# Kernel optimization log

Hardware: AMD Instinct MI355X
Metric: run time of the kernel (lower is better)

Reference implementation:

```python
import jax, jax.numpy as jnp
import numpy as np

B, S, D, H, FF = 1, 2048, 2048, 32, 8192
HD = D // H
SCALING = HD ** -0.5
WBITS, ABITS = 8, 8
NEG = jnp.finfo(jnp.float32).min


def ste_round(x):
    # straight-through estimator round
    return x + jax.lax.stop_gradient(jnp.round(x) - x)


def fake_quant(x, bits, axis):
    # min-max asymmetric fake quantization (OmniQuant-style dynamic quant)
    qmax = float(2 ** bits - 1)
    xmin = jnp.minimum(jnp.min(x, axis=axis, keepdims=True), 0.0)
    xmax = jnp.maximum(jnp.max(x, axis=axis, keepdims=True), 0.0)
    scale = jnp.maximum((xmax - xmin) / qmax, 1e-5)
    zp = jnp.round(-xmin / scale)
    q = jnp.clip(ste_round(x / scale) + zp, 0.0, qmax)
    return (q - zp) * scale


def qlinear(x, W, b):
    # QuantLinear: quantize activation per-token, weight per-output-channel
    xq = fake_quant(x, ABITS, -1)
    Wq = fake_quant(W, WBITS, 1)  # W: [out, in], per-row (output channel)
    return xq @ Wq.T + b


def layernorm(x, g, b):
    mu = jnp.mean(x, axis=-1, keepdims=True)
    var = jnp.var(x, axis=-1, keepdims=True)
    return (x - mu) * jax.lax.rsqrt(var + 1e-5) * g + b


def setup_inputs():
    key = jax.random.key(0)
    ks = jax.random.split(key, 16)
    w = lambda k, shape: (jax.random.normal(k, shape) * 0.02).astype(jnp.float32)
    hidden_states = jax.random.normal(ks[0], (B, S, D), dtype=jnp.float32)
    causal = jnp.tril(jnp.ones((S, S), dtype=bool))
    attention_mask = jnp.where(causal, 0.0, NEG)[None, None].astype(jnp.float32)
    attention_mask = jnp.broadcast_to(attention_mask, (B, 1, S, S))
    return {
        'hidden_states': hidden_states,
        'attention_mask': attention_mask,
        'Wq': w(ks[1], (D, D)), 'bq': jnp.zeros((D,), jnp.float32),
        'Wk': w(ks[2], (D, D)), 'bk': jnp.zeros((D,), jnp.float32),
        'Wv': w(ks[3], (D, D)), 'bv': jnp.zeros((D,), jnp.float32),
        'Wo': w(ks[4], (D, D)), 'bo': jnp.zeros((D,), jnp.float32),
        'ln1_g': jnp.ones((D,), jnp.float32), 'ln1_b': jnp.zeros((D,), jnp.float32),
        'W1': w(ks[5], (FF, D)), 'b1': jnp.zeros((FF,), jnp.float32),
        'W2': w(ks[6], (D, FF)), 'b2': jnp.zeros((D,), jnp.float32),
        'ln2_g': jnp.ones((D,), jnp.float32), 'ln2_b': jnp.zeros((D,), jnp.float32),
    }


def _split_heads(x):
    # [B,S,D] -> [B,H,S,HD]
    return x.reshape(B, S, H, HD).transpose(0, 2, 1, 3)


def _layer(hidden_states, attention_mask, Wq, bq, Wk, bk, Wv, bv, Wo, bo,
           ln1_g, ln1_b, W1, b1, W2, b2, ln2_g, ln2_b):
    # ---- self attention block (do_layer_norm_before=True) ----
    residual = hidden_states
    x = layernorm(hidden_states, ln1_g, ln1_b)

    q = qlinear(x, Wq, bq) * SCALING
    q = fake_quant(q, ABITS, -1)          # qkt_matmul.quant_x1
    k = qlinear(x, Wk, bk)
    k = fake_quant(k, ABITS, -1)          # qkt_matmul.quant_x2
    v = qlinear(x, Wv, bv)
    v = fake_quant(v, ABITS, -1)          # pv_matmul.quant_x2

    qh, kh, vh = _split_heads(q), _split_heads(k), _split_heads(v)
    scores = jnp.einsum('bhqd,bhkd->bhqk', qh, kh)  # [B,H,S,S]
    scores = scores + attention_mask
    scores = jnp.maximum(scores, NEG)
    probs = jax.nn.softmax(scores, axis=-1)
    probs = fake_quant(probs, ABITS, -1)  # pv_matmul.quant_x1
    ctx = jnp.einsum('bhqk,bhkd->bhqd', probs, vh)
    ctx = ctx.transpose(0, 2, 1, 3).reshape(B, S, D)
    attn_out = qlinear(ctx, Wo, bo)
    hidden_states = residual + attn_out

    # ---- FFN block ----
    residual = hidden_states
    x = layernorm(hidden_states, ln2_g, ln2_b)
    x = jax.nn.relu(qlinear(x, W1, b1))
    x = qlinear(x, W2, b2)
    return residual + x


def reference(hidden_states, attention_mask, Wq, bq, Wk, bk, Wv, bv, Wo, bo,
              ln1_g, ln1_b, W1, b1, W2, b2, ln2_g, ln2_b):
    return _layer(hidden_states, attention_mask, Wq, bq, Wk, bk, Wv, bv, Wo, bo,
                  ln1_g, ln1_b, W1, b1, W2, b2, ln2_g, ln2_b)
```

## Files before the change

kernel.cpp:

```cpp
#include <hip/hip_runtime.h>
#include <hip/hip_bf16.h>
#include <math.h>

#define S_LEN 2048
#define D_DIM 2048
#define H_NUM 32
#define HD_DIM 64
#define FF_DIM 8192
#define QMAX 255.0f
#define LOG2E 1.4426950408889634f

typedef __attribute__((ext_vector_type(4))) float f32x4;
typedef __attribute__((ext_vector_type(4))) int i32x4;
typedef __attribute__((ext_vector_type(8))) __bf16 bf16x8;
typedef unsigned short u16;
typedef signed char i8;

__device__ __forceinline__ u16 f32i_to_bf16(float v) {
  return (u16)(__float_as_uint(v) >> 16);
}
__device__ __forceinline__ u16 f32_to_bf16_rne(float v) {
  __bf16 b = (__bf16)v;
  return *(u16*)&b;
}
__device__ __forceinline__ float bf16_to_f32(u16 u) {
  return __uint_as_float((unsigned int)u << 16);
}
__device__ __forceinline__ int pack4_i8(float q0, float q1, float q2, float q3) {
  int c0 = (int)q0 - 128, c1 = (int)q1 - 128, c2 = (int)q2 - 128, c3 = (int)q3 - 128;
  return (c0 & 0xFF) | ((c1 & 0xFF) << 8) | ((c2 & 0xFF) << 16) | ((c3 & 0xFF) << 24);
}

__device__ __forceinline__ float wred_sum(float v) {
#pragma unroll
  for (int o = 1; o < 64; o <<= 1) v += __shfl_xor(v, o, 64);
  return v;
}
__device__ __forceinline__ float wred_min(float v) {
#pragma unroll
  for (int o = 1; o < 64; o <<= 1) v = fminf(v, __shfl_xor(v, o, 64));
  return v;
}
__device__ __forceinline__ float wred_max(float v) {
#pragma unroll
  for (int o = 1; o < 64; o <<= 1) v = fmaxf(v, __shfl_xor(v, o, 64));
  return v;
}

__device__ __forceinline__ void gload_lds16(const void* g, void* l) {
  __builtin_amdgcn_global_load_lds(
      (__attribute__((address_space(1))) void*)(g),
      (__attribute__((address_space(3))) void*)(l), 16, 0, 0);
}

__device__ __forceinline__ void xcd_swz(int& bx, int& by) {
  const int gy = gridDim.y;
  const int nwg = gridDim.x * gy;
  const int orig = blockIdx.y + gy * blockIdx.x;
  const int swz = (orig & 7) * (nwg >> 3) + (orig >> 3);
  by = swz % gy;
  bx = swz / gy;
}

__device__ __forceinline__ void attn_map(int bid, int& h, int& ti) {
  h = bid & (H_NUM - 1);
  const int a = (bid >> 5) & 7;
  const int b = bid >> 8;
  ti = (b == 0) ? (31 - a) : (b == 1) ? a : (b == 2) ? (23 - a) : (8 + a);
}

__global__ __launch_bounds__(256) void ln_quant_i8(const float* __restrict__ x,
                                                   const float* __restrict__ g,
                                                   const float* __restrict__ bvec,
                                                   i8* __restrict__ out,
                                                   float* __restrict__ srow,
                                                   float* __restrict__ zrow,
                                                   float* __restrict__ S0row,
                                                   float* __restrict__ S1row) {
  __shared__ float red[8];
  const int row = blockIdx.x, tid = threadIdx.x;
  const float4* xr = (const float4*)(x + (size_t)row * D_DIM);
  const float4* g4 = (const float4*)g;
  const float4* b4 = (const float4*)bvec;

  float4 v0 = xr[tid], v1 = xr[tid + 256];
  float s = v0.x + v0.y + v0.z + v0.w + v1.x + v1.y + v1.z + v1.w;
  float ss = v0.x * v0.x + v0.y * v0.y + v0.z * v0.z + v0.w * v0.w +
             v1.x * v1.x + v1.y * v1.y + v1.z * v1.z + v1.w * v1.w;
  s = wred_sum(s); ss = wred_sum(ss);
  if ((tid & 63) == 0) { red[tid >> 6] = s; red[4 + (tid >> 6)] = ss; }
  __syncthreads();
  float mu = (red[0] + red[1] + red[2] + red[3]) / (float)D_DIM;
  float var = (red[4] + red[5] + red[6] + red[7]) / (float)D_DIM - mu * mu;
  float rstd = 1.0f / sqrtf(var + 1e-5f);
  __syncthreads();

  float mn = 0.f, mx = 0.f;
  float4 n0, n1;
  {
    float4 gg = g4[tid], bb = b4[tid];
    n0.x = (v0.x - mu) * rstd * gg.x + bb.x; n0.y = (v0.y - mu) * rstd * gg.y + bb.y;
    n0.z = (v0.z - mu) * rstd * gg.z + bb.z; n0.w = (v0.w - mu) * rstd * gg.w + bb.w;
    gg = g4[tid + 256]; bb = b4[tid + 256];
    n1.x = (v1.x - mu) * rstd * gg.x + bb.x; n1.y = (v1.y - mu) * rstd * gg.y + bb.y;
    n1.z = (v1.z - mu) * rstd * gg.z + bb.z; n1.w = (v1.w - mu) * rstd * gg.w + bb.w;
    mn = fminf(mn, fminf(fminf(n0.x, n0.y), fminf(n0.z, n0.w)));
    mn = fminf(mn, fminf(fminf(n1.x, n1.y), fminf(n1.z, n1.w)));
    mx = fmaxf(mx, fmaxf(fmaxf(n0.x, n0.y), fmaxf(n0.z, n0.w)));
    mx = fmaxf(mx, fmaxf(fmaxf(n1.x, n1.y), fmaxf(n1.z, n1.w)));
  }
  mn = wred_min(mn); mx = wred_max(mx);
  if ((tid & 63) == 0) { red[tid >> 6] = mn; red[4 + (tid >> 6)] = mx; }
  __syncthreads();
  mn = fminf(fminf(red[0], red[1]), fminf(red[2], red[3]));
  mx = fmaxf(fmaxf(red[4], red[5]), fmaxf(red[6], red[7]));
  float scale = fmaxf((mx - mn) / QMAX, 1e-5f);
  float zp = rintf(-mn / scale);
  if (tid == 0) { srow[row] = scale; zrow[row] = 128.0f - zp; }

  float q00 = fminf(fmaxf(rintf(n0.x / scale) + zp, 0.f), QMAX);
  float q01 = fminf(fmaxf(rintf(n0.y / scale) + zp, 0.f), QMAX);
  float q02 = fminf(fmaxf(rintf(n0.z / scale) + zp, 0.f), QMAX);
  float q03 = fminf(fmaxf(rintf(n0.w / scale) + zp, 0.f), QMAX);
  float q10 = fminf(fmaxf(rintf(n1.x / scale) + zp, 0.f), QMAX);
  float q11 = fminf(fmaxf(rintf(n1.y / scale) + zp, 0.f), QMAX);
  float q12 = fminf(fmaxf(rintf(n1.z / scale) + zp, 0.f), QMAX);
  float q13 = fminf(fmaxf(rintf(n1.w / scale) + zp, 0.f), QMAX);
  *(int*)&out[(size_t)row * D_DIM + tid * 4] = pack4_i8(q00, q01, q02, q03);
  *(int*)&out[(size_t)row * D_DIM + 1024 + tid * 4] = pack4_i8(q10, q11, q12, q13);
  float s0 = q00 + q01 + q02 + q03 - 512.f;
  float s1 = q10 + q11 + q12 + q13 - 512.f;
  __syncthreads();
  s0 = wred_sum(s0); s1 = wred_sum(s1);
  if ((tid & 63) == 0) { red[tid >> 6] = s0; red[4 + (tid >> 6)] = s1; }
  __syncthreads();
  if (tid == 0) {
    S0row[row] = red[0] + red[1] + red[2] + red[3];
    S1row[row] = red[4] + red[5] + red[6] + red[7];
  }
}

__global__ __launch_bounds__(256) void act_quant_i8(const float* __restrict__ x,
                                                    i8* __restrict__ out,
                                                    float* __restrict__ srow,
                                                    float* __restrict__ zrow,
                                                    float* __restrict__ S0row,
                                                    float* __restrict__ S1row) {
  __shared__ float red[8];
  const int row = blockIdx.x, tid = threadIdx.x;
  const float4* xr = (const float4*)(x + (size_t)row * D_DIM);
  float4 n0 = xr[tid], n1 = xr[tid + 256];
  float mn = 0.f, mx = 0.f;
  mn = fminf(mn, fminf(fminf(n0.x, n0.y), fminf(n0.z, n0.w)));
  mn = fminf(mn, fminf(fminf(n1.x, n1.y), fminf(n1.z, n1.w)));
  mx = fmaxf(mx, fmaxf(fmaxf(n0.x, n0.y), fmaxf(n0.z, n0.w)));
  mx = fmaxf(mx, fmaxf(fmaxf(n1.x, n1.y), fmaxf(n1.z, n1.w)));
  mn = wred_min(mn); mx = wred_max(mx);
  if ((tid & 63) == 0) { red[tid >> 6] = mn; red[4 + (tid >> 6)] = mx; }
  __syncthreads();
  mn = fminf(fminf(red[0], red[1]), fminf(red[2], red[3]));
  mx = fmaxf(fmaxf(red[4], red[5]), fmaxf(red[6], red[7]));
  float scale = fmaxf((mx - mn) / QMAX, 1e-5f);
  float zp = rintf(-mn / scale);
  if (tid == 0) { srow[row] = scale; zrow[row] = 128.0f - zp; }
  float q00 = fminf(fmaxf(rintf(n0.x / scale) + zp, 0.f), QMAX);
  float q01 = fminf(fmaxf(rintf(n0.y / scale) + zp, 0.f), QMAX);
  float q02 = fminf(fmaxf(rintf(n0.z / scale) + zp, 0.f), QMAX);
  float q03 = fminf(fmaxf(rintf(n0.w / scale) + zp, 0.f), QMAX);
  float q10 = fminf(fmaxf(rintf(n1.x / scale) + zp, 0.f), QMAX);
  float q11 = fminf(fmaxf(rintf(n1.y / scale) + zp, 0.f), QMAX);
  float q12 = fminf(fmaxf(rintf(n1.z / scale) + zp, 0.f), QMAX);
  float q13 = fminf(fmaxf(rintf(n1.w / scale) + zp, 0.f), QMAX);
  *(int*)&out[(size_t)row * D_DIM + tid * 4] = pack4_i8(q00, q01, q02, q03);
  *(int*)&out[(size_t)row * D_DIM + 1024 + tid * 4] = pack4_i8(q10, q11, q12, q13);
  float s0 = q00 + q01 + q02 + q03 - 512.f;
  float s1 = q10 + q11 + q12 + q13 - 512.f;
  __syncthreads();
  s0 = wred_sum(s0); s1 = wred_sum(s1);
  if ((tid & 63) == 0) { red[tid >> 6] = s0; red[4 + (tid >> 6)] = s1; }
  __syncthreads();
  if (tid == 0) {
    S0row[row] = red[0] + red[1] + red[2] + red[3];
    S1row[row] = red[4] + red[5] + red[6] + red[7];
  }
}

__device__ __forceinline__ void wquantD_body(const float* __restrict__ wr0,
                                             i8* __restrict__ wo,
                                             float* __restrict__ sc,
                                             float* __restrict__ zc,
                                             float* __restrict__ S0c,
                                             float* __restrict__ S1c, int row) {
  __shared__ float red[8];
  const int tid = threadIdx.x;
  const float4* wr = (const float4*)wr0;
  float4 v0 = wr[tid], v1 = wr[tid + 256];
  float mn = 0.f, mx = 0.f;
  mn = fminf(mn, fminf(fminf(v0.x, v0.y), fminf(v0.z, v0.w)));
  mn = fminf(mn, fminf(fminf(v1.x, v1.y), fminf(v1.z, v1.w)));
  mx = fmaxf(mx, fmaxf(fmaxf(v0.x, v0.y), fmaxf(v0.z, v0.w)));
  mx = fmaxf(mx, fmaxf(fmaxf(v1.x, v1.y), fmaxf(v1.z, v1.w)));
  mn = wred_min(mn); mx = wred_max(mx);
  if ((tid & 63) == 0) { red[tid >> 6] = mn; red[4 + (tid >> 6)] = mx; }
  __syncthreads();
  mn = fminf(fminf(red[0], red[1]), fminf(red[2], red[3]));
  mx = fmaxf(fmaxf(red[4], red[5]), fmaxf(red[6], red[7]));
  float scale = fmaxf((mx - mn) / QMAX, 1e-5f);
  float zp = rintf(-mn / scale);
  if (tid == 0) { sc[row] = scale; zc[row] = 128.0f - zp; }
  float q00 = fminf(fmaxf(rintf(v0.x / scale) + zp, 0.f), QMAX);
  float q01 = fminf(fmaxf(rintf(v0.y / scale) + zp, 0.f), QMAX);
  float q02 = fminf(fmaxf(rintf(v0.z / scale) + zp, 0.f), QMAX);
  float q03 = fminf(fmaxf(rintf(v0.w / scale) + zp, 0.f), QMAX);
  float q10 = fminf(fmaxf(rintf(v1.x / scale) + zp, 0.f), QMAX);
  float q11 = fminf(fmaxf(rintf(v1.y / scale) + zp, 0.f), QMAX);
  float q12 = fminf(fmaxf(rintf(v1.z / scale) + zp, 0.f), QMAX);
  float q13 = fminf(fmaxf(rintf(v1.w / scale) + zp, 0.f), QMAX);
  *(int*)&wo[tid * 4] = pack4_i8(q00, q01, q02, q03);
  *(int*)&wo[1024 + tid * 4] = pack4_i8(q10, q11, q12, q13);
  float s0 = q00 + q01 + q02 + q03 - 512.f;
  float s1 = q10 + q11 + q12 + q13 - 512.f;
  __syncthreads();
  s0 = wred_sum(s0); s1 = wred_sum(s1);
  if ((tid & 63) == 0) { red[tid >> 6] = s0; red[4 + (tid >> 6)] = s1; }
  __syncthreads();
  if (tid == 0) {
    S0c[row] = red[0] + red[1] + red[2] + red[3];
    S1c[row] = red[4] + red[5] + red[6] + red[7];
  }
}

__global__ __launch_bounds__(256) void wquantD_i8(
    const float* __restrict__ Wq, i8* __restrict__ Oq, float* sq_, float* zq_, float* aq_, float* bq_,
    const float* __restrict__ Wk, i8* __restrict__ Ok, float* sk_, float* zk_, float* ak_, float* bk_,
    const float* __restrict__ Wv, i8* __restrict__ Ov, float* sv_, float* zv_, float* av_, float* bv_,
    const float* __restrict__ Wo, i8* __restrict__ Oo, float* so_, float* zo_, float* ao_, float* bo_,
    const float* __restrict__ W1, i8* __restrict__ O1, float* s1_, float* z1_, float* a1_, float* b1_) {
  const int b = blockIdx.x;
  int which, row;
  if (b < 4 * D_DIM) { which = b >> 11; row = b & (D_DIM - 1); }
  else { which = 4; row = b - 4 * D_DIM; }
  const float* W = (which == 0) ? Wq : (which == 1) ? Wk : (which == 2) ? Wv : (which == 3) ? Wo : W1;
  i8* O = (which == 0) ? Oq : (which == 1) ? Ok : (which == 2) ? Ov : (which == 3) ? Oo : O1;
  float* sc = (which == 0) ? sq_ : (which == 1) ? sk_ : (which == 2) ? sv_ : (which == 3) ? so_ : s1_;
  float* zc = (which == 0) ? zq_ : (which == 1) ? zk_ : (which == 2) ? zv_ : (which == 3) ? zo_ : z1_;
  float* Sa = (which == 0) ? aq_ : (which == 1) ? ak_ : (which == 2) ? av_ : (which == 3) ? ao_ : a1_;
  float* Sb = (which == 0) ? bq_ : (which == 1) ? bk_ : (which == 2) ? bv_ : (which == 3) ? bo_ : b1_;
  wquantD_body(W + (size_t)row * D_DIM, O + (size_t)row * D_DIM, sc, zc, Sa, Sb, row);
}

__global__ __launch_bounds__(256) void wquantW2_i8(const float* __restrict__ W,
                                                   i8* __restrict__ Wi,
                                                   float* __restrict__ sc,
                                                   float* __restrict__ zc,
                                                   float* __restrict__ S0c,
                                                   float* __restrict__ S1c) {
  __shared__ float red[8];
  const int row = blockIdx.x, tid = threadIdx.x;
  const float4* wr = (const float4*)(W + (size_t)row * FF_DIM);
  float4 v[8];
#pragma unroll
  for (int j = 0; j < 8; ++j) v[j] = wr[tid + 256 * j];
  float mn = 0.f, mx = 0.f;
#pragma unroll
  for (int j = 0; j < 8; ++j) {
    mn = fminf(mn, fminf(fminf(v[j].x, v[j].y), fminf(v[j].z, v[j].w)));
    mx = fmaxf(mx, fmaxf(fmaxf(v[j].x, v[j].y), fmaxf(v[j].z, v[j].w)));
  }
  mn = wred_min(mn); mx = wred_max(mx);
  if ((tid & 63) == 0) { red[tid >> 6] = mn; red[4 + (tid >> 6)] = mx; }
  __syncthreads();
  mn = fminf(fminf(red[0], red[1]), fminf(red[2], red[3]));
  mx = fmaxf(fmaxf(red[4], red[5]), fmaxf(red[6], red[7]));
  float scale = fmaxf((mx - mn) / QMAX, 1e-5f);
  float zp = rintf(-mn / scale);
  if (tid == 0) { sc[row] = scale; zc[row] = 128.0f - zp; }
  float s0 = 0.f, s1 = 0.f;
#pragma unroll
  for (int j = 0; j < 8; ++j) {
    float q0 = fminf(fmaxf(rintf(v[j].x / scale) + zp, 0.f), QMAX);
    float q1 = fminf(fmaxf(rintf(v[j].y / scale) + zp, 0.f), QMAX);
    float q2 = fminf(fmaxf(rintf(v[j].z / scale) + zp, 0.f), QMAX);
    float q3 = fminf(fmaxf(rintf(v[j].w / scale) + zp, 0.f), QMAX);
    *(int*)&Wi[(size_t)row * FF_DIM + (tid + 256 * j) * 4] = pack4_i8(q0, q1, q2, q3);
    float gs = q0 + q1 + q2 + q3 - 512.f;
    if (j < 4) s0 += gs; else s1 += gs;
  }
  __syncthreads();
  s0 = wred_sum(s0); s1 = wred_sum(s1);
  if ((tid & 63) == 0) { red[tid >> 6] = s0; red[4 + (tid >> 6)] = s1; }
  __syncthreads();
  if (tid == 0) {
    S0c[row] = red[0] + red[1] + red[2] + red[3];
    S1c[row] = red[4] + red[5] + red[6] + red[7];
  }
}

__global__ __launch_bounds__(256) void requant3(
    const u16* __restrict__ qv, const float* __restrict__ tqmn, const float* __restrict__ tqmx,
    u16* __restrict__ qo, float* __restrict__ sqv,
    const u16* __restrict__ kv, const float* __restrict__ tkmn, const float* __restrict__ tkmx,
    u16* __restrict__ ko, float* __restrict__ skv,
    const u16* __restrict__ vv, const float* __restrict__ tvmn, const float* __restrict__ tvmx,
    u16* __restrict__ vo) {
// ... 314 lines not shown
    const int col = col0 + ni * 16;
#pragma unroll
    for (int mi = 0; mi < 4; ++mi)
#pragma unroll
      for (int r = 0; r < 4; ++r)
        dst[(size_t)(rbase + mi * 16 + r) * D_DIM + col] = (float)acc[mi][ni][r];
  }
}

__global__ __launch_bounds__(256) void splitk_reduce4(
    const float* __restrict__ part,
    const float* __restrict__ sxa, const float* __restrict__ zxa,
    const float* __restrict__ Sxa0, const float* __restrict__ Sxa1,
    const float* __restrict__ sw, const float* __restrict__ zw,
    const float* __restrict__ Sw0, const float* __restrict__ Sw1,
    float Kf, const float* __restrict__ bias, const float* __restrict__ res,
    float* __restrict__ out) {
  const size_t st4 = (size_t)S_LEN * D_DIM / 4;
  for (size_t i = (size_t)blockIdx.x * 256 + threadIdx.x; i < st4;
       i += (size_t)gridDim.x * 256) {
    const int row = (int)(i >> 9);
    const int c4 = (int)(i & 511);
    float4 s = ((const float4*)part)[i];
    float4 p1 = ((const float4*)part)[i + st4];
    float4 p2 = ((const float4*)part)[i + 2 * st4];
    float4 p3 = ((const float4*)part)[i + 3 * st4];
    s.x += p1.x + p2.x + p3.x; s.y += p1.y + p2.y + p3.y;
    s.z += p1.z + p2.z + p3.z; s.w += p1.w + p2.w + p3.w;
    const float sxr = sxa[row], zxr = zxa[row];
    const float Sxr = Sxa0[row] + Sxa1[row];
    float4 ws = ((const float4*)sw)[c4];
    float4 wz = ((const float4*)zw)[c4];
    float4 w0 = ((const float4*)Sw0)[c4];
    float4 w1 = ((const float4*)Sw1)[c4];
    float4 b4 = ((const float4*)bias)[c4];
    float4 o;
    o.x = sxr * ws.x * (s.x + zxr * (w0.x + w1.x) + wz.x * Sxr + Kf * zxr * wz.x) + b4.x;
    o.y = sxr * ws.y * (s.y + zxr * (w0.y + w1.y) + wz.y * Sxr + Kf * zxr * wz.y) + b4.y;
    o.z = sxr * ws.z * (s.z + zxr * (w0.z + w1.z) + wz.z * Sxr + Kf * zxr * wz.z) + b4.z;
    o.w = sxr * ws.w * (s.w + zxr * (w0.w + w1.w) + wz.w * Sxr + Kf * zxr * wz.w) + b4.w;
    if (res) {
      float4 r = ((const float4*)res)[i];
      o.x += r.x; o.y += r.y; o.z += r.z; o.w += r.w;
    }
    ((float4*)out)[i] = o;
  }
}

__global__ __launch_bounds__(256) void splitk_reduce_ln(
    const float* __restrict__ part,
    const float* __restrict__ sxa, const float* __restrict__ zxa,
    const float* __restrict__ Sxa0, const float* __restrict__ Sxa1,
    const float* __restrict__ sw, const float* __restrict__ zw,
    const float* __restrict__ Sw0, const float* __restrict__ Sw1,
    const float* __restrict__ bias, const float* __restrict__ res,
    float* __restrict__ h2out,
    const float* __restrict__ g, const float* __restrict__ bvec,
    i8* __restrict__ out, float* __restrict__ srow, float* __restrict__ zrow,
    float* __restrict__ S0row, float* __restrict__ S1row) {
  __shared__ float red[8];
  const int row = blockIdx.x, tid = threadIdx.x;
  const size_t st = (size_t)S_LEN * D_DIM;
  const float4* p0 = (const float4*)(part + (size_t)row * D_DIM);
  const float4* p1 = (const float4*)(part + st + (size_t)row * D_DIM);
  const float4* p2 = (const float4*)(part + 2 * st + (size_t)row * D_DIM);
  const float4* p3 = (const float4*)(part + 3 * st + (size_t)row * D_DIM);
  const float4* rr = (const float4*)(res + (size_t)row * D_DIM);
  const float4* b4 = (const float4*)bias;
  const float4* g4 = (const float4*)g;
  const float4* e4 = (const float4*)bvec;

  const float sxr = sxa[row], zxr = zxa[row];
  const float Sxr = Sxa0[row] + Sxa1[row];

  float4 v0, v1;
#pragma unroll
  for (int h = 0; h < 2; ++h) {
    const int idx = tid + h * 256;
    float4 a = p0[idx], q = p1[idx], u = p2[idx], w = p3[idx];
    float4 ws = ((const float4*)sw)[idx];
    float4 wz = ((const float4*)zw)[idx];
    float4 s0 = ((const float4*)Sw0)[idx];
    float4 s1 = ((const float4*)Sw1)[idx];
    float4 bb = b4[idx], rv = rr[idx];
    float4 o;
    o.x = sxr * ws.x * (a.x + q.x + u.x + w.x + zxr * (s0.x + s1.x) + wz.x * Sxr + 2048.0f * zxr * wz.x) + bb.x + rv.x;
    o.y = sxr * ws.y * (a.y + q.y + u.y + w.y + zxr * (s0.y + s1.y) + wz.y * Sxr + 2048.0f * zxr * wz.y) + bb.y + rv.y;
    o.z = sxr * ws.z * (a.z + q.z + u.z + w.z + zxr * (s0.z + s1.z) + wz.z * Sxr + 2048.0f * zxr * wz.z) + bb.z + rv.z;
    o.w = sxr * ws.w * (a.w + q.w + u.w + w.w + zxr * (s0.w + s1.w) + wz.w * Sxr + 2048.0f * zxr * wz.w) + bb.w + rv.w;
    if (h == 0) v0 = o; else v1 = o;
  }
  float* h2r = h2out + (size_t)row * D_DIM;
  *(float4*)&h2r[tid * 4] = v0;
  *(float4*)&h2r[1024 + tid * 4] = v1;

  float s = v0.x + v0.y + v0.z + v0.w + v1.x + v1.y + v1.z + v1.w;
  float ss = v0.x * v0.x + v0.y * v0.y + v0.z * v0.z + v0.w * v0.w +
             v1.x * v1.x + v1.y * v1.y + v1.z * v1.z + v1.w * v1.w;
  s = wred_sum(s); ss = wred_sum(ss);
  if ((tid & 63) == 0) { red[tid >> 6] = s; red[4 + (tid >> 6)] = ss; }
  __syncthreads();
  float mu = (red[0] + red[1] + red[2] + red[3]) / (float)D_DIM;
  float var = (red[4] + red[5] + red[6] + red[7]) / (float)D_DIM - mu * mu;
  float rstd = 1.0f / sqrtf(var + 1e-5f);
  __syncthreads();

  float mn = 0.f, mx = 0.f;
  float4 n0, n1;
  {
    float4 gg = g4[tid], bb = e4[tid];
    n0.x = (v0.x - mu) * rstd * gg.x + bb.x; n0.y = (v0.y - mu) * rstd * gg.y + bb.y;
    n0.z = (v0.z - mu) * rstd * gg.z + bb.z; n0.w = (v0.w - mu) * rstd * gg.w + bb.w;
    gg = g4[tid + 256]; bb = e4[tid + 256];
    n1.x = (v1.x - mu) * rstd * gg.x + bb.x; n1.y = (v1.y - mu) * rstd * gg.y + bb.y;
    n1.z = (v1.z - mu) * rstd * gg.z + bb.z; n1.w = (v1.w - mu) * rstd * gg.w + bb.w;
    mn = fminf(mn, fminf(fminf(n0.x, n0.y), fminf(n0.z, n0.w)));
    mn = fminf(mn, fminf(fminf(n1.x, n1.y), fminf(n1.z, n1.w)));
    mx = fmaxf(mx, fmaxf(fmaxf(n0.x, n0.y), fmaxf(n0.z, n0.w)));
    mx = fmaxf(mx, fmaxf(fmaxf(n1.x, n1.y), fmaxf(n1.z, n1.w)));
  }
  mn = wred_min(mn); mx = wred_max(mx);
  if ((tid & 63) == 0) { red[tid >> 6] = mn; red[4 + (tid >> 6)] = mx; }
  __syncthreads();
  mn = fminf(fminf(red[0], red[1]), fminf(red[2], red[3]));
  mx = fmaxf(fmaxf(red[4], red[5]), fmaxf(red[6], red[7]));
  float scale = fmaxf((mx - mn) / QMAX, 1e-5f);
  float zp = rintf(-mn / scale);
  if (tid == 0) { srow[row] = scale; zrow[row] = 128.0f - zp; }
  float q00 = fminf(fmaxf(rintf(n0.x / scale) + zp, 0.f), QMAX);
  float q01 = fminf(fmaxf(rintf(n0.y / scale) + zp, 0.f), QMAX);
  float q02 = fminf(fmaxf(rintf(n0.z / scale) + zp, 0.f), QMAX);
  float q03 = fminf(fmaxf(rintf(n0.w / scale) + zp, 0.f), QMAX);
  float q10 = fminf(fmaxf(rintf(n1.x / scale) + zp, 0.f), QMAX);
  float q11 = fminf(fmaxf(rintf(n1.y / scale) + zp, 0.f), QMAX);
  float q12 = fminf(fmaxf(rintf(n1.z / scale) + zp, 0.f), QMAX);
  float q13 = fminf(fmaxf(rintf(n1.w / scale) + zp, 0.f), QMAX);
  *(int*)&out[(size_t)row * D_DIM + tid * 4] = pack4_i8(q00, q01, q02, q03);
  *(int*)&out[(size_t)row * D_DIM + 1024 + tid * 4] = pack4_i8(q10, q11, q12, q13);
  float s0 = q00 + q01 + q02 + q03 - 512.f;
  float s1 = q10 + q11 + q12 + q13 - 512.f;
  __syncthreads();
  s0 = wred_sum(s0); s1 = wred_sum(s1);
  if ((tid & 63) == 0) { red[tid >> 6] = s0; red[4 + (tid >> 6)] = s1; }
  __syncthreads();
  if (tid == 0) {
    S0row[row] = red[0] + red[1] + red[2] + red[3];
    S1row[row] = red[4] + red[5] + red[6] + red[7];
  }
}

__global__ __launch_bounds__(256) void attn_ml(
    const u16* __restrict__ qi, const float* __restrict__ sq,
    const u16* __restrict__ ki, const float* __restrict__ sk,
    float* __restrict__ Mb, float* __restrict__ Lb) {
  __shared__ __align__(16) u16 Ks[64][72];
  int h, ti; attn_map(blockIdx.x, h, ti);
  const int i0 = ti * 64;
  const int tid = threadIdx.x;
  const int wid = tid >> 6, lane = tid & 63;
  const int lr = lane & 15, g = lane >> 4;
  const size_t hbase = (size_t)h * HD_DIM;

  const int r_a = tid >> 3, ch_a = tid & 7;
  const int r_b = 32 + r_a;

  const bf16x8 aq0 = *(const bf16x8*)&qi[(size_t)(i0 + wid * 16 + lr) * D_DIM + hbase + g * 8];
  const bf16x8 aq1 = *(const bf16x8*)&qi[(size_t)(i0 + wid * 16 + lr) * D_DIM + hbase + 32 + g * 8];
  float sq2[4];
#pragma unroll
  for (int r = 0; r < 4; ++r) sq2[r] = sq[i0 + wid * 16 + g * 4 + r] * LOG2E;

  const int ntiles = i0 / 64 + 1;
  float m_r[4] = {-1e30f, -1e30f, -1e30f, -1e30f};
  float l_r[4] = {0.f, 0.f, 0.f, 0.f};

  float4 ka0 = *(const float4*)&ki[(size_t)r_a * D_DIM + hbase + ch_a * 8];
  float4 ka1 = *(const float4*)&ki[(size_t)r_b * D_DIM + hbase + ch_a * 8];
  for (int t = 0; t < ntiles; ++t) {
    __syncthreads();
    *(float4*)&Ks[r_a][ch_a * 8] = ka0;
    *(float4*)&Ks[r_b][ch_a * 8] = ka1;
    __syncthreads();
    if (t + 1 < ntiles) {
      const int jn = (t + 1) * 64;
      ka0 = *(const float4*)&ki[(size_t)(jn + r_a) * D_DIM + hbase + ch_a * 8];
      ka1 = *(const float4*)&ki[(size_t)(jn + r_b) * D_DIM + hbase + ch_a * 8];
    }

    f32x4 accs[4] = {};
#pragma unroll
    for (int ni = 0; ni < 4; ++ni) {
      bf16x8 b0 = *(const bf16x8*)&Ks[ni * 16 + lr][g * 8];
      bf16x8 b1 = *(const bf16x8*)&Ks[ni * 16 + lr][32 + g * 8];
      accs[ni] = __builtin_amdgcn_mfma_f32_16x16x32_bf16(aq0, b0, accs[ni], 0, 0, 0);
      accs[ni] = __builtin_amdgcn_mfma_f32_16x16x32_bf16(aq1, b1, accs[ni], 0, 0, 0);
    }

    const int jt = t * 64;
    float tv[4][4];
#pragma unroll
    for (int ni = 0; ni < 4; ++ni) {
      const float skc = sk[jt + ni * 16 + lr];
#pragma unroll
      for (int r = 0; r < 4; ++r) tv[ni][r] = accs[ni][r] * sq2[r] * skc;
    }
    if (t == ntiles - 1) {
      const int jcol = jt + lr, irow = i0 + wid * 16 + g * 4;
#pragma unroll
      for (int ni = 0; ni < 4; ++ni)
#pragma unroll
        for (int r = 0; r < 4; ++r)
          if (jcol + ni * 16 > irow + r) tv[ni][r] = -1e30f;
    }
#pragma unroll
    for (int r = 0; r < 4; ++r) {
      float tmax = fmaxf(fmaxf(tv[0][r], tv[1][r]), fmaxf(tv[2][r], tv[3][r]));
      tmax = fmaxf(tmax, __shfl_xor(tmax, 1, 64));
      tmax = fmaxf(tmax, __shfl_xor(tmax, 2, 64));
      tmax = fmaxf(tmax, __shfl_xor(tmax, 4, 64));
      tmax = fmaxf(tmax, __shfl_xor(tmax, 8, 64));
      float mnew = fmaxf(m_r[r], tmax);
      float sum = exp2f(tv[0][r] - mnew) + exp2f(tv[1][r] - mnew) +
                  exp2f(tv[2][r] - mnew) + exp2f(tv[3][r] - mnew);
      sum += __shfl_xor(sum, 1, 64);
      sum += __shfl_xor(sum, 2, 64);
      sum += __shfl_xor(sum, 4, 64);
      sum += __shfl_xor(sum, 8, 64);
      l_r[r] = l_r[r] * exp2f(m_r[r] - mnew) + sum;
      m_r[r] = mnew;
    }
  }

  if (lr == 0) {
#pragma unroll
    for (int r = 0; r < 4; ++r) {
      const int row = i0 + wid * 16 + g * 4 + r;
      Mb[(size_t)h * S_LEN + row] = m_r[r];
      Lb[(size_t)h * S_LEN + row] = l_r[r];
    }
  }
}

__global__ __launch_bounds__(256) void attn_pv(
    const u16* __restrict__ qi, const float* __restrict__ sq,
    const u16* __restrict__ ki, const float* __restrict__ sk,
    const u16* __restrict__ vt,
    const float* __restrict__ Mb, const float* __restrict__ Lb,
    float* __restrict__ ctx) {
  __shared__ __align__(16) u16 Ks[64][72];
  __shared__ __align__(16) u16 Ps[64][72];
  __shared__ __align__(16) u16 Vt[64][72];
  int h, ti; attn_map(blockIdx.x, h, ti);
  const int i0 = ti * 64;
  const int tid = threadIdx.x;
  const int wid = tid >> 6, lane = tid & 63;
  const int lr = lane & 15, g = lane >> 4;
  const size_t hbase = (size_t)h * HD_DIM;
  const size_t vtbase = (size_t)h * HD_DIM * S_LEN;

  const int r_a = tid >> 3, ch_a = tid & 7;
  const int r_b = 32 + r_a;

  const bf16x8 aq0 = *(const bf16x8*)&qi[(size_t)(i0 + wid * 16 + lr) * D_DIM + hbase + g * 8];
  const bf16x8 aq1 = *(const bf16x8*)&qi[(size_t)(i0 + wid * 16 + lr) * D_DIM + hbase + 32 + g * 8];

  float sq2[4], b_r[4], qsc[4];
#pragma unroll
  for (int r = 0; r < 4; ++r) {
    const int row = i0 + wid * 16 + g * 4 + r;
    sq2[r] = sq[row] * LOG2E;
    float m_t = Mb[(size_t)h * S_LEN + row];
    float li = Lb[(size_t)h * S_LEN + row];
    float sc = fmaxf((1.0f / li) / QMAX, 1e-5f);
    qsc[r] = sc;
    b_r[r] = m_t - log2f(1.0f / (li * sc));
  }

  const int ntiles = i0 / 64 + 1;
  f32x4 acco[4] = {};
  float4 kb0 = *(const float4*)&ki[(size_t)r_a * D_DIM + hbase + ch_a * 8];
  float4 kb1 = *(const float4*)&ki[(size_t)r_b * D_DIM + hbase + ch_a * 8];
  float4 vb0 = *(const float4*)&vt[vtbase + (size_t)r_a * S_LEN + ch_a * 8];
  float4 vb1 = *(const float4*)&vt[vtbase + (size_t)r_b * S_LEN + ch_a * 8];
  for (int t = 0; t < ntiles; ++t) {
    __syncthreads();
    *(float4*)&Ks[r_a][ch_a * 8] = kb0;
    *(float4*)&Ks[r_b][ch_a * 8] = kb1;
    *(float4*)&Vt[r_a][ch_a * 8] = vb0;
    *(float4*)&Vt[r_b][ch_a * 8] = vb1;
    __syncthreads();
    if (t + 1 < ntiles) {
      const int jn = (t + 1) * 64;
      kb0 = *(const float4*)&ki[(size_t)(jn + r_a) * D_DIM + hbase + ch_a * 8];
      kb1 = *(const float4*)&ki[(size_t)(jn + r_b) * D_DIM + hbase + ch_a * 8];
      vb0 = *(const float4*)&vt[vtbase + (size_t)r_a * S_LEN + jn + ch_a * 8];
      vb1 = *(const float4*)&vt[vtbase + (size_t)r_b * S_LEN + jn + ch_a * 8];
    }

    f32x4 accs[4] = {};
#pragma unroll
    for (int ni = 0; ni < 4; ++ni) {
      bf16x8 b0 = *(const bf16x8*)&Ks[ni * 16 + lr][g * 8];
      bf16x8 b1 = *(const bf16x8*)&Ks[ni * 16 + lr][32 + g * 8];
      accs[ni] = __builtin_amdgcn_mfma_f32_16x16x32_bf16(aq0, b0, accs[ni], 0, 0, 0);
      accs[ni] = __builtin_amdgcn_mfma_f32_16x16x32_bf16(aq1, b1, accs[ni], 0, 0, 0);
    }

    const int jt = t * 64;
    const bool diag = (t == ntiles - 1);
    const int jcol = jt + lr, irow = i0 + wid * 16 + g * 4;
#pragma unroll
    for (int ni = 0; ni < 4; ++ni) {
      const float skc = sk[jt + ni * 16 + lr];
#pragma unroll
      for (int r = 0; r < 4; ++r) {
        float tvv = accs[ni][r] * sq2[r] * skc;
        if (diag && (jcol + ni * 16 > irow + r)) tvv = -1e30f;
        float q8 = fminf(rintf(exp2f(tvv - b_r[r])), QMAX);
        Ps[wid * 16 + g * 4 + r][ni * 16 + lr] = f32i_to_bf16(q8);
      }
    }

    bf16x8 ap0 = *(const bf16x8*)&Ps[wid * 16 + lr][g * 8];
    bf16x8 ap1 = *(const bf16x8*)&Ps[wid * 16 + lr][32 + g * 8];
#pragma unroll
    for (int ni = 0; ni < 4; ++ni) {
      bf16x8 b0 = *(const bf16x8*)&Vt[ni * 16 + lr][g * 8];
      bf16x8 b1 = *(const bf16x8*)&Vt[ni * 16 + lr][32 + g * 8];
      acco[ni] = __builtin_amdgcn_mfma_f32_16x16x32_bf16(ap0, b0, acco[ni], 0, 0, 0);
      acco[ni] = __builtin_amdgcn_mfma_f32_16x16x32_bf16(ap1, b1, acco[ni], 0, 0, 0);
    }
  }

#pragma unroll
  for (int ni = 0; ni < 4; ++ni)
#pragma unroll
    for (int r = 0; r < 4; ++r) {
      const int row = i0 + wid * 16 + g * 4 + r;
      ctx[(size_t)row * D_DIM + hbase + ni * 16 + lr] = acco[ni][r] * qsc[r];
    }
}

extern "C" void kernel_launch(void* const* d_in, const int* in_sizes, int n_in,
                              void* d_out, int out_size, void* d_ws, size_t ws_size,
                              hipStream_t stream) {
  (void)in_sizes; (void)n_in; (void)out_size;
  const float* hs  = (const float*)d_in[0];
  const float* Wq  = (const float*)d_in[2];
  const float* bq  = (const float*)d_in[3];
  const float* Wk  = (const float*)d_in[4];
  const float* bk  = (const float*)d_in[5];
  const float* Wv  = (const float*)d_in[6];
  const float* bv  = (const float*)d_in[7];
  const float* Wo  = (const float*)d_in[8];
  const float* bo  = (const float*)d_in[9];
  const float* g1  = (const float*)d_in[10];
  const float* be1 = (const float*)d_in[11];
  const float* W1  = (const float*)d_in[12];
  const float* bf1 = (const float*)d_in[13];
  const float* W2  = (const float*)d_in[14];
  const float* bf2 = (const float*)d_in[15];
  const float* g2  = (const float*)d_in[16];
  const float* be2 = (const float*)d_in[17];
  float* out = (float*)d_out;

  const size_t SD = (size_t)S_LEN * D_DIM;
  const size_t SF = (size_t)S_LEN * FF_DIM;
  const size_t HS = (size_t)H_NUM * S_LEN;

  char* p = (char*)d_ws;
  auto alloc = [&](size_t bytes) { char* r = p; p += (bytes + 255) & ~(size_t)255; return r; };

  float* h2   = (float*)alloc(SD * 4);
  float* sx   = (float*)alloc(S_LEN * 4);
  float* zx   = (float*)alloc(S_LEN * 4);
  float* Sx0  = (float*)alloc(S_LEN * 4);
  float* Sx1  = (float*)alloc(S_LEN * 4);
  float* sy   = (float*)alloc(S_LEN * 4);
  float* zy   = (float*)alloc(S_LEN * 4);
  float* Sy0  = (float*)alloc(S_LEN * 4);
  float* Sy1  = (float*)alloc(S_LEN * 4);
  float* sxf  = (float*)alloc(S_LEN * 4);
  float* zxf  = (float*)alloc(S_LEN * 4);
  float* Sf0  = (float*)alloc(S_LEN * 4);
  float* Sf1  = (float*)alloc(S_LEN * 4);
  float* sqv  = (float*)alloc(S_LEN * 4);
  float* skv  = (float*)alloc(S_LEN * 4);
  float* Mb   = (float*)alloc(HS * 4);
  float* Lbv  = (float*)alloc(HS * 4);
  float* swq = (float*)alloc(D_DIM * 4); float* zwq = (float*)alloc(D_DIM * 4);
  float* Sq0 = (float*)alloc(D_DIM * 4); float* Sq1 = (float*)alloc(D_DIM * 4);
  float* swk = (float*)alloc(D_DIM * 4); float* zwk = (float*)alloc(D_DIM * 4);
  float* Sk0 = (float*)alloc(D_DIM * 4); float* Sk1 = (float*)alloc(D_DIM * 4);
  float* swv = (float*)alloc(D_DIM * 4); float* zwv = (float*)alloc(D_DIM * 4);
  float* Sv0 = (float*)alloc(D_DIM * 4); float* Sv1 = (float*)alloc(D_DIM * 4);
  float* swo = (float*)alloc(D_DIM * 4); float* zwo = (float*)alloc(D_DIM * 4);
  float* So0 = (float*)alloc(D_DIM * 4); float* So1 = (float*)alloc(D_DIM * 4);
  float* sw1 = (float*)alloc(FF_DIM * 4); float* zw1 = (float*)alloc(FF_DIM * 4);
  float* S10 = (float*)alloc(FF_DIM * 4); float* S11 = (float*)alloc(FF_DIM * 4);
  float* sw2 = (float*)alloc(D_DIM * 4); float* zw2 = (float*)alloc(D_DIM * 4);
  float* S20 = (float*)alloc(D_DIM * 4); float* S21 = (float*)alloc(D_DIM * 4);
  float* tqmn = (float*)alloc(S_LEN * 32 * 4);
  float* tqmx = (float*)alloc(S_LEN * 32 * 4);
  float* tkmn = (float*)alloc(S_LEN * 32 * 4);
  float* tkmx = (float*)alloc(S_LEN * 32 * 4);
  float* tvmn = (float*)alloc(S_LEN * 32 * 4);
  float* tvmx = (float*)alloc(S_LEN * 32 * 4);
  float* tf1x = (float*)alloc(S_LEN * 128 * 4);
  i8* xi  = (i8*)alloc(SD);
  i8* wqi = (i8*)alloc(SD);
  i8* wki = (i8*)alloc(SD);
  i8* wvi = (i8*)alloc(SD);
  i8* woi = (i8*)alloc(SD);
  i8* w1i = (i8*)alloc(SF);
  i8* w2i = (i8*)alloc(SF);
  i8* f1i = (i8*)alloc(SF);
  char* arena = alloc(8 * SD * 2);
  u16* qv   = (u16*)arena;
  u16* kv   = qv + SD;
  u16* vv   = kv + SD;
  u16* qi8  = vv + SD;
  u16* ki8  = qi8 + SD;
  u16* vfb  = ki8 + SD;
  float* ctxb = (float*)(vfb + SD);
  u16* vtb  = qv;
  float* pwo = (float*)arena;
  u16* f1v = (u16*)arena;
  float* pw2 = (float*)arena;
  size_t need = (size_t)(p - (char*)d_ws);
  if (ws_size < need) return;

  dim3 blk(256);

  wquantD_i8<<<4 * D_DIM + FF_DIM, blk, 0, stream>>>(
      Wq, wqi, swq, zwq, Sq0, Sq1,
      Wk, wki, swk, zwk, Sk0, Sk1,
      Wv, wvi, swv, zwv, Sv0, Sv1,
      Wo, woi, swo, zwo, So0, So1,
      W1, w1i, sw1, zw1, S10, S11);
  wquantW2_i8<<<D_DIM, blk, 0, stream>>>(W2, w2i, sw2, zw2, S20, S21);

  ln_quant_i8<<<S_LEN, blk, 0, stream>>>(hs, g1, be1, xi, sx, zx, Sx0, Sx1);

  dim3 gqkv(3 * D_DIM / 128, S_LEN / 128);
  gemm_qkv_i8<<<gqkv, blk, 0, stream>>>(xi, sx, zx, Sx0, Sx1,
                                        wqi, swq, zwq, Sq0, Sq1, bq, qv, tqmn, tqmx,
                                        wki, swk, zwk, Sk0, Sk1, bk, kv, tkmn, tkmx,
                                        wvi, swv, zwv, Sv0, Sv1, bv, vv, tvmn, tvmx);

  requant3<<<3 * S_LEN, blk, 0, stream>>>(qv, tqmn, tqmx, qi8, sqv,
                                          kv, tkmn, tkmx, ki8, skv,
                                          vv, tvmn, tvmx, vfb);

  dim3 gtv(S_LEN / 64, H_NUM);
  transpose_v<<<gtv, blk, 0, stream>>>(vfb, vtb);

  const int ga = (S_LEN / 64) * H_NUM;
  attn_ml<<<ga, blk, 0, stream>>>(qi8, sqv, ki8, skv, Mb, Lbv);
  attn_pv<<<ga, blk, 0, stream>>>(qi8, sqv, ki8, skv, vtb, Mb, Lbv, ctxb);

  act_quant_i8<<<S_LEN, blk, 0, stream>>>(ctxb, xi, sx, zx, Sx0, Sx1);

  dim3 gwo(D_DIM / 128, S_LEN / 128, 4);
  gemm_splitk_i8<<<gwo, blk, 0, stream>>>(xi, woi, pwo, D_DIM, 4);
  splitk_reduce_ln<<<S_LEN, blk, 0, stream>>>(pwo, sx, zx, Sx0, Sx1,
                                              swo, zwo, So0, So1, bo, hs, h2,
                                              g2, be2, xi, sy, zy, Sy0, Sy1);

  dim3 gff(FF_DIM / 128, S_LEN / 128);
  gemm_w1_i8<<<gff, blk, 0, stream>>>(xi, sy, zy, Sy0, Sy1,
                                      w1i, sw1, zw1, S10, S11, bf1, f1v, tf1x);
  requant_ff_i8<<<S_LEN, blk, 0, stream>>>(f1v, tf1x, f1i, sxf, zxf, Sf0, Sf1);

  dim3 gw2(D_DIM / 128, S_LEN / 128, 4);
  gemm_splitk_i8<<<gw2, blk, 0, stream>>>(f1i, w2i, pw2, FF_DIM, 4);
  splitk_reduce4<<<2048, blk, 0, stream>>>(pw2, sxf, zxf, Sf0, Sf1,
                                           sw2, zw2, S20, S21, (float)FF_DIM,
                                           bf2, h2, out);
}
```

Baseline: 402.3 us.

## Split causal attention key range into chunks to balance long query tiles

Query tiles are now split along the key dimension into 1-4 chunks depending on their causal length, so attention launches 2560 blocks of roughly equal work instead of 1024 uneven ones. Each chunk writes its partial max and sum, and the PV pass merges all chunk statistics to get the global softmax normalisation. The per-chunk partial context outputs are summed inside the following activation-quant kernel. This trades extra partial-buffer memory traffic and a larger workspace for better load balance and occupancy during attention.

After: 404.7 us. Within noise of the previous version (+0.6%).

```diff
diff --git a/kernel.cpp b/kernel.cpp
--- a/kernel.cpp
+++ b/kernel.cpp
@@ -62,11 +62,14 @@
   bx = swz / gy;
 }
 
-__device__ __forceinline__ void attn_map(int bid, int& h, int& ti) {
+__device__ __forceinline__ void attn_map_chunk(int bid, int& h, int& ti,
+                                               int& c, int& nc) {
   h = bid & (H_NUM - 1);
-  const int a = (bid >> 5) & 7;
-  const int b = bid >> 8;
-  ti = (b == 0) ? (31 - a) : (b == 1) ? a : (b == 2) ? (23 - a) : (8 + a);
+  const int idx = 79 - (bid >> 5);
+  if (idx < 8)       { ti = idx;                 c = 0;              nc = 1; }
+  else if (idx < 24) { ti = 8 + ((idx - 8) >> 1);  c = (idx - 8) & 1;  nc = 2; }
+  else if (idx < 48) { ti = 16 + (idx - 24) / 3;   c = (idx - 24) % 3; nc = 3; }
+  else               { ti = 24 + ((idx - 48) >> 2); c = (idx - 48) & 3; nc = 4; }
 }
 
 __global__ __launch_bounds__(256) void ln_quant_i8(const float* __restrict__ x,
@@ -140,16 +143,36 @@
   }
 }
 
-__global__ __launch_bounds__(256) void act_quant_i8(const float* __restrict__ x,
-                                                    i8* __restrict__ out,
-                                                    float* __restrict__ srow,
-                                                    float* __restrict__ zrow,
-                                                    float* __restrict__ S0row,
-                                                    float* __restrict__ S1row) {
+__global__ __launch_bounds__(256) void act_quant_i8(
+    const float* __restrict__ c0p, const float* __restrict__ c1p,
+    const float* __restrict__ c2p, const float* __restrict__ c3p,
+    i8* __restrict__ out,
+    float* __restrict__ srow, float* __restrict__ zrow,
+    float* __restrict__ S0row, float* __restrict__ S1row) {
   __shared__ float red[8];
   const int row = blockIdx.x, tid = threadIdx.x;
-  const float4* xr = (const float4*)(x + (size_t)row * D_DIM);
-  float4 n0 = xr[tid], n1 = xr[tid + 256];
+  const int nc = (row >> 9) + 1;
+  const size_t base = (size_t)row * D_DIM;
+  float4 n0 = *(const float4*)(c0p + base + tid * 4);
+  float4 n1 = *(const float4*)(c0p + base + 1024 + tid * 4);
+  if (nc > 1) {
+    float4 a = *(const float4*)(c1p + base + tid * 4);
+    float4 b = *(const float4*)(c1p + base + 1024 + tid * 4);
+    n0.x += a.x; n0.y += a.y; n0.z += a.z; n0.w += a.w;
+    n1.x += b.x; n1.y += b.y; n1.z += b.z; n1.w += b.w;
+  }
+  if (nc > 2) {
+    float4 a = *(const float4*)(c2p + base + tid * 4);
+    float4 b = *(const float4*)(c2p + base + 1024 + tid * 4);
+    n0.x += a.x; n0.y += a.y; n0.z += a.z; n0.w += a.w;
+    n1.x += b.x; n1.y += b.y; n1.z += b.z; n1.w += b.w;
+  }
+  if (nc > 3) {
+    float4 a = *(const float4*)(c3p + base + tid * 4);
+    float4 b = *(const float4*)(c3p + base + 1024 + tid * 4);
+    n0.x += a.x; n0.y += a.y; n0.z += a.z; n0.w += a.w;
+    n1.x += b.x; n1.y += b.y; n1.z += b.z; n1.w += b.w;
+  }
   float mn = 0.f, mx = 0.f;
   mn = fminf(mn, fminf(fminf(n0.x, n0.y), fminf(n0.z, n0.w)));
   mn = fminf(mn, fminf(fminf(n1.x, n1.y), fminf(n1.z, n1.w)));
@@ -770,10 +793,12 @@
 __global__ __launch_bounds__(256) void attn_ml(
     const u16* __restrict__ qi, const float* __restrict__ sq,
     const u16* __restrict__ ki, const float* __restrict__ sk,
-    float* __restrict__ Mb, float* __restrict__ Lb) {
+    float* __restrict__ Mp, float* __restrict__ Lp) {
   __shared__ __align__(16) u16 Ks[64][72];
-  int h, ti; attn_map(blockIdx.x, h, ti);
+  int h, ti, c, nc; attn_map_chunk(blockIdx.x, h, ti, c, nc);
   const int i0 = ti * 64;
+  const int nt = ti + 1;
+  const int j0t = (c * nt) / nc, j1t = ((c + 1) * nt) / nc;
   const int tid = threadIdx.x;
   const int wid = tid >> 6, lane = tid & 63;
   const int lr = lane & 15, g = lane >> 4;
@@ -788,18 +813,17 @@
 #pragma unroll
   for (int r = 0; r < 4; ++r) sq2[r] = sq[i0 + wid * 16 + g * 4 + r] * LOG2E;
 
-  const int ntiles = i0 / 64 + 1;
   float m_r[4] = {-1e30f, -1e30f, -1e30f, -1e30f};
   float l_r[4] = {0.f, 0.f, 0.f, 0.f};
 
-  float4 ka0 = *(const float4*)&ki[(size_t)r_a * D_DIM + hbase + ch_a * 8];
-  float4 ka1 = *(const float4*)&ki[(size_t)r_b * D_DIM + hbase + ch_a * 8];
-  for (int t = 0; t < ntiles; ++t) {
+  float4 ka0 = *(const float4*)&ki[(size_t)(j0t * 64 + r_a) * D_DIM + hbase + ch_a * 8];
+  float4 ka1 = *(const float4*)&ki[(size_t)(j0t * 64 + r_b) * D_DIM + hbase + ch_a * 8];
+  for (int t = j0t; t < j1t; ++t) {
     __syncthreads();
     *(float4*)&Ks[r_a][ch_a * 8] = ka0;
     *(float4*)&Ks[r_b][ch_a * 8] = ka1;
     __syncthreads();
-    if (t + 1 < ntiles) {
+    if (t + 1 < j1t) {
       const int jn = (t + 1) * 64;
       ka0 = *(const float4*)&ki[(size_t)(jn + r_a) * D_DIM + hbase + ch_a * 8];
       ka1 = *(const float4*)&ki[(size_t)(jn + r_b) * D_DIM + hbase + ch_a * 8];
@@ -822,7 +846,7 @@
 #pragma unroll
       for (int r = 0; r < 4; ++r) tv[ni][r] = accs[ni][r] * sq2[r] * skc;
     }
-    if (t == ntiles - 1) {
+    if (t == nt - 1) {
       const int jcol = jt + lr, irow = i0 + wid * 16 + g * 4;
 #pragma unroll
       for (int ni = 0; ni < 4; ++ni)
@@ -850,11 +874,12 @@
   }
 
   if (lr == 0) {
+    const size_t slot = (size_t)c * H_NUM * S_LEN + (size_t)h * S_LEN;
 #pragma unroll
     for (int r = 0; r < 4; ++r) {
       const int row = i0 + wid * 16 + g * 4 + r;
-      Mb[(size_t)h * S_LEN + row] = m_r[r];
-      Lb[(size_t)h * S_LEN + row] = l_r[r];
+      Mp[slot + row] = m_r[r];
+      Lp[slot + row] = l_r[r];
     }
   }
 }
@@ -863,18 +888,22 @@
     const u16* __restrict__ qi, const float* __restrict__ sq,
     const u16* __restrict__ ki, const float* __restrict__ sk,
     const u16* __restrict__ vt,
-    const float* __restrict__ Mb, const float* __restrict__ Lb,
-    float* __restrict__ ctx) {
+    const float* __restrict__ Mp, const float* __restrict__ Lp,
+    float* __restrict__ c0p, float* __restrict__ c1p,
+    float* __restrict__ c2p, float* __restrict__ c3p) {
   __shared__ __align__(16) u16 Ks[64][72];
   __shared__ __align__(16) u16 Ps[64][72];
   __shared__ __align__(16) u16 Vt[64][72];
-  int h, ti; attn_map(blockIdx.x, h, ti);
+  int h, ti, c, nc; attn_map_chunk(blockIdx.x, h, ti, c, nc);
   const int i0 = ti * 64;
+  const int nt = ti + 1;
+  const int j0t = (c * nt) / nc, j1t = ((c + 1) * nt) / nc;
   const int tid = threadIdx.x;
   const int wid = tid >> 6, lane = tid & 63;
   const int lr = lane & 15, g = lane >> 4;
   const size_t hbase = (size_t)h * HD_DIM;
   const size_t vtbase = (size_t)h * HD_DIM * S_LEN;
+  float* ctxp = (c == 0) ? c0p : (c == 1) ? c1p : (c == 2) ? c2p : c3p;
 
   const int r_a = tid >> 3, ch_a = tid & 7;
   const int r_b = 32 + r_a;
@@ -882,32 +911,41 @@
   const bf16x8 aq0 = *(const bf16x8*)&qi[(size_t)(i0 + wid * 16 + lr) * D_DIM + hbase + g * 8];
   const bf16x8 aq1 = *(const bf16x8*)&qi[(size_t)(i0 + wid * 16 + lr) * D_DIM + hbase + 32 + g * 8];
 
+  const size_t HS = (size_t)H_NUM * S_LEN;
   float sq2[4], b_r[4], qsc[4];
 #pragma unroll
   for (int r = 0; r < 4; ++r) {
     const int row = i0 + wid * 16 + g * 4 + r;
     sq2[r] = sq[row] * LOG2E;
-    float m_t = Mb[(size_t)h * S_LEN + row];
-    float li = Lb[(size_t)h * S_LEN + row];
-    float sc = fmaxf((1.0f / li) / QMAX, 1e-5f);
+    float m = Mp[(size_t)h * S_LEN + row];
+    float L0 = Lp[(size_t)h * S_LEN + row];
+    float m1 = (nc > 1) ? Mp[HS + (size_t)h * S_LEN + row] : -1e30f;
+    float L1 = (nc > 1) ? Lp[HS + (size_t)h * S_LEN + row] : 0.f;
+    float m2 = (nc > 2) ? Mp[2 * HS + (size_t)h * S_LEN + row] : -1e30f;
+    float L2 = (nc > 2) ? Lp[2 * HS + (size_t)h * S_LEN + row] : 0.f;
+    float m3 = (nc > 3) ? Mp[3 * HS + (size_t)h * S_LEN + row] : -1e30f;
+    float L3 = (nc > 3) ? Lp[3 * HS + (size_t)h * S_LEN + row] : 0.f;
+    float mg = fmaxf(fmaxf(m, m1), fmaxf(m2, m3));
+    float L = L0 * exp2f(m - mg) + L1 * exp2f(m1 - mg) +
+              L2 * exp2f(m2 - mg) + L3 * exp2f(m3 - mg);
+    float sc = fmaxf((1.0f / L) / QMAX, 1e-5f);
     qsc[r] = sc;
-    b_r[r] = m_t - log2f(1.0f / (li * sc));
-  }
-
-  const int ntiles = i0 / 64 + 1;
+    b_r[r] = mg - log2f(1.0f / (L * sc));
+  }
+
   f32x4 acco[4] = {};
-  float4 kb0 = *(const float4*)&ki[(size_t)r_a * D_DIM + hbase + ch_a * 8];
-  float4 kb1 = *(const float4*)&ki[(size_t)r_b * D_DIM + hbase + ch_a * 8];
-  float4 vb0 = *(const float4*)&vt[vtbase + (size_t)r_a * S_LEN + ch_a * 8];
-  float4 vb1 = *(const float4*)&vt[vtbase + (size_t)r_b * S_LEN + ch_a * 8];
-  for (int t = 0; t < ntiles; ++t) {
+  float4 kb0 = *(const float4*)&ki[(size_t)(j0t * 64 + r_a) * D_DIM + hbase + ch_a * 8];
+  float4 kb1 = *(const float4*)&ki[(size_t)(j0t * 64 + r_b) * D_DIM + hbase + ch_a * 8];
+  float4 vb0 = *(const float4*)&vt[vtbase + (size_t)r_a * S_LEN + j0t * 64 + ch_a * 8];
+  float4 vb1 = *(const float4*)&vt[vtbase + (size_t)r_b * S_LEN + j0t * 64 + ch_a * 8];
+  for (int t = j0t; t < j1t; ++t) {
     __syncthreads();
     *(float4*)&Ks[r_a][ch_a * 8] = kb0;
     *(float4*)&Ks[r_b][ch_a * 8] = kb1;
     *(float4*)&Vt[r_a][ch_a * 8] = vb0;
     *(float4*)&Vt[r_b][ch_a * 8] = vb1;
     __syncthreads();
-    if (t + 1 < ntiles) {
+    if (t + 1 < j1t) {
       const int jn = (t + 1) * 64;
       kb0 = *(const float4*)&ki[(size_t)(jn + r_a) * D_DIM + hbase + ch_a * 8];
       kb1 = *(const float4*)&ki[(size_t)(jn + r_b) * D_DIM + hbase + ch_a * 8];
@@ -925,7 +963,7 @@
     }
 
     const int jt = t * 64;
-    const bool diag = (t == ntiles - 1);
+    const bool diag = (t == nt - 1);
     const int jcol = jt + lr, irow = i0 + wid * 16 + g * 4;
 #pragma unroll
     for (int ni = 0; ni < 4; ++ni) {
@@ -955,7 +993,7 @@
 #pragma unroll
     for (int r = 0; r < 4; ++r) {
       const int row = i0 + wid * 16 + g * 4 + r;
-      ctx[(size_t)row * D_DIM + hbase + ni * 16 + lr] = acco[ni][r] * qsc[r];
+      ctxp[(size_t)row * D_DIM + hbase + ni * 16 + lr] = acco[ni][r] * qsc[r];
     }
 }
 
@@ -1004,8 +1042,8 @@
   float* Sf1  = (float*)alloc(S_LEN * 4);
   float* sqv  = (float*)alloc(S_LEN * 4);
   float* skv  = (float*)alloc(S_LEN * 4);
-  float* Mb   = (float*)alloc(HS * 4);
-  float* Lbv  = (float*)alloc(HS * 4);
+  float* Mp   = (float*)alloc(4 * HS * 4);
+  float* Lp   = (float*)alloc(4 * HS * 4);
   float* swq = (float*)alloc(D_DIM * 4); float* zwq = (float*)alloc(D_DIM * 4);
   float* Sq0 = (float*)alloc(D_DIM * 4); float* Sq1 = (float*)alloc(D_DIM * 4);
   float* swk = (float*)alloc(D_DIM * 4); float* zwk = (float*)alloc(D_DIM * 4);
@@ -1033,18 +1071,21 @@
   i8* w1i = (i8*)alloc(SF);
   i8* w2i = (i8*)alloc(SF);
   i8* f1i = (i8*)alloc(SF);
-  char* arena = alloc(8 * SD * 2);
+  char* arena = alloc(12 * SD * 2);
   u16* qv   = (u16*)arena;
   u16* kv   = qv + SD;
   u16* vv   = kv + SD;
   u16* qi8  = vv + SD;
   u16* ki8  = qi8 + SD;
   u16* vfb  = ki8 + SD;
-  float* ctxb = (float*)(vfb + SD);
   u16* vtb  = qv;
+  float* ctx0 = (float*)(arena + 1 * SD * 2);
+  float* ctx1 = (float*)(arena + 6 * SD * 2);
+  float* ctx2 = (float*)(arena + 8 * SD * 2);
+  float* ctx3 = (float*)(arena + 10 * SD * 2);
   float* pwo = (float*)arena;
   u16* f1v = (u16*)arena;
-  float* pw2 = (float*)arena;
+  float* pw2 = (float*)(arena + 4 * SD * 2);
   size_t need = (size_t)(p - (char*)d_ws);
   if (ws_size < need) return;
 
@@ -1073,11 +1114,13 @@
   dim3 gtv(S_LEN / 64, H_NUM);
   transpose_v<<<gtv, blk, 0, stream>>>(vfb, vtb);
 
-  const int ga = (S_LEN / 64) * H_NUM;
-  attn_ml<<<ga, blk, 0, stream>>>(qi8, sqv, ki8, skv, Mb, Lbv);
-  attn_pv<<<ga, blk, 0, stream>>>(qi8, sqv, ki8, skv, vtb, Mb, Lbv, ctxb);
-
-  act_quant_i8<<<S_LEN, blk, 0, stream>>>(ctxb, xi, sx, zx, Sx0, Sx1);
+  const int ga = 2560;
+  attn_ml<<<ga, blk, 0, stream>>>(qi8, sqv, ki8, skv, Mp, Lp);
+  attn_pv<<<ga, blk, 0, stream>>>(qi8, sqv, ki8, skv, vtb, Mp, Lp,
+                                  ctx0, ctx1, ctx2, ctx3);
+
+  act_quant_i8<<<S_LEN, blk, 0, stream>>>(ctx0, ctx1, ctx2, ctx3,
+                                          xi, sx, zx, Sx0, Sx1);
 
   dim3 gwo(D_DIM / 128, S_LEN / 128, 4);
   gemm_splitk_i8<<<gwo, blk, 0, stream>>>(xi, woi, pwo, D_DIM, 4);
```
